# Kernel optimization log

Hardware: AMD Instinct MI355X
Metric: run time of the kernel (lower is better)

Reference implementation:

```python
import jax, jax.numpy as jnp
import numpy as np

N_NODES = 50000
N_EDGES = 400000
D_IN = 128
D_H = 128
N_CLASSES = 20
N_GRAPHS = 256
EPS_BN = 1e-5


def _lin_params(key, d_in, d_out, scale=0.05):
    kw, kb = jax.random.split(key)
    W = jax.random.normal(kw, (d_in, d_out), jnp.float32) * scale
    b = jax.random.normal(kb, (d_out,), jnp.float32) * scale
    return W, b


def setup_inputs() -> dict:
    key = jax.random.key(0)
    ks = jax.random.split(key, 20)
    inp = {
        "x": jax.random.normal(ks[0], (N_NODES, D_IN), jnp.float32),
        "edge_index": jax.random.randint(ks[1], (2, N_EDGES), 0, N_NODES, jnp.int32),
        "batch": jnp.sort(jax.random.randint(ks[2], (N_NODES,), 0, N_GRAPHS, jnp.int32)),
    }
    kidx = 3
    for li, d_in in zip((1, 2, 3), (D_IN, D_H, D_H)):
        for nm in ("q", "k", "v", "s"):
            W, b = _lin_params(ks[kidx], d_in, D_H)
            kidx += 1
            inp[f"W{nm}{li}"] = W
            inp[f"b{nm}{li}"] = b
        inp[f"gamma{li}"] = jnp.ones((D_H,), jnp.float32)
        inp[f"beta{li}"] = jnp.zeros((D_H,), jnp.float32)
    Wl, bl = _lin_params(ks[kidx], D_H, N_CLASSES)
    inp["Wlin"] = Wl
    inp["blin"] = bl
    return inp


def _segment_softmax(logits, seg, n):
    m = jax.ops.segment_max(logits, seg, num_segments=n)
    e = jnp.exp(logits - m[seg])
    s = jax.ops.segment_sum(e, seg, num_segments=n)
    return e / (s[seg] + 1e-16)


def _transformer_conv(x, src, dst, Wq, bq, Wk, bk, Wv, bv, Ws, bs):
    # heads=1, concat=True, root_weight=True (PyG TransformerConv defaults)
    q = x @ Wq + bq  # [N, d]
    k = x @ Wk + bk
    v = x @ Wv + bv
    d = q.shape[-1]
    logits = jnp.sum(q[dst] * k[src], axis=-1) / jnp.sqrt(jnp.float32(d))  # [E]
    alpha = _segment_softmax(logits, dst, x.shape[0])
    out = jax.ops.segment_sum(alpha[:, None] * v[src], dst, num_segments=x.shape[0])
    return out + x @ Ws + bs


def _batch_norm(x, gamma, beta):
    mu = jnp.mean(x, axis=0)
    var = jnp.var(x, axis=0)
    return gamma * (x - mu) * jax.lax.rsqrt(var + EPS_BN) + beta


def _global_mean_pool(x, batch, n_graphs):
    sums = jax.ops.segment_sum(x, batch, num_segments=n_graphs)
    cnt = jax.ops.segment_sum(jnp.ones((x.shape[0],), x.dtype), batch, num_segments=n_graphs)
    return sums / jnp.maximum(cnt, 1.0)[:, None]


def reference(x, edge_index, batch,
              Wq1, bq1, Wk1, bk1, Wv1, bv1, Ws1, bs1, gamma1, beta1,
              Wq2, bq2, Wk2, bk2, Wv2, bv2, Ws2, bs2, gamma2, beta2,
              Wq3, bq3, Wk3, bk3, Wv3, bv3, Ws3, bs3, gamma3, beta3,
              Wlin, blin):
    src, dst = edge_index[0], edge_index[1]
    h = _transformer_conv(x, src, dst, Wq1, bq1, Wk1, bk1, Wv1, bv1, Ws1, bs1)
    h = jax.nn.relu(_batch_norm(h, gamma1, beta1))  # dropout inactive (eval)
    h = _transformer_conv(h, src, dst, Wq2, bq2, Wk2, bk2, Wv2, bv2, Ws2, bs2)
    h = jax.nn.relu(_batch_norm(h, gamma2, beta2))
    h = _transformer_conv(h, src, dst, Wq3, bq3, Wk3, bk3, Wv3, bv3, Ws3, bs3)
    h = jax.nn.relu(_batch_norm(h, gamma3, beta3))
    g = _global_mean_pool(h, batch, N_GRAPHS)  # [G, d]
    return g @ Wlin + blin  # [G, num_classes]
```

## Files before the change

### kernel.cpp

```cpp
#include <hip/hip_runtime.h>

#define N_NODES 50000
#define N_EDGES 400000
#define DH 128
#define N_GRAPHS 256

#define SCAN_CHUNK 512
#define N_CHUNKS ((N_NODES + SCAN_CHUNK - 1) / SCAN_CHUNK)
#define ATTN_BLOCKS ((N_NODES + 15) / 16)

typedef __bf16 bf16x8 __attribute__((ext_vector_type(8)));
typedef float f32x4 __attribute__((ext_vector_type(4)));
typedef _Float16 f16x2 __attribute__((ext_vector_type(2)));
typedef _Float16 f16x8 __attribute__((ext_vector_type(8)));

#define DEV __device__ __forceinline__

#if defined(__has_builtin)
#if __has_builtin(__builtin_amdgcn_fdot2)
#define HAS_FDOT2 1
#endif
#endif

DEV float fdot2acc(f16x2 a, f16x2 b, float c) {
#ifdef HAS_FDOT2
  return __builtin_amdgcn_fdot2(a, b, c, false);
#else
  return (float)a.x * (float)b.x + (float)a.y * (float)b.y + c;
#endif
}

DEV unsigned short f2bf(float f) {
  union { float f; unsigned int i; } v; v.f = f;
  unsigned int x = v.i;
  unsigned int r = (x + 0x7fffu + ((x >> 16) & 1u)) >> 16;
  return (unsigned short)r;
}

struct WPtrs { const float* w[12]; };

__global__ void repack_kernel(WPtrs wp, unsigned short* __restrict__ WB) {
  int mat = blockIdx.y;
  int m = blockIdx.x * 256 + threadIdx.x;
  int j = m & 7;
  int lane = (m >> 3) & 63;
  int ct = (m >> 9) & 7;
  int kk = m >> 12;
  int i = kk * 32 + (lane >> 4) * 8 + j;
  int o = ct * 16 + (lane & 15);
  WB[mat * 16384 + m] = f2bf(wp.w[mat][i * 128 + o]);
}

__global__ void deg_count(const int* __restrict__ ei, int* __restrict__ deg, int E) {
  int e = blockIdx.x * 256 + threadIdx.x;
  if (e < E) atomicAdd(&deg[ei[E + e]], 1);
}

__global__ __launch_bounds__(256) void scan_sum(const int* __restrict__ deg,
                                                int* __restrict__ partials, int N) {
  __shared__ int red[256];
  int b = blockIdx.x, t = threadIdx.x;
  int base = b * SCAN_CHUNK + t * 2;
  int s = 0;
  if (base + 1 < N) { int2 v = *reinterpret_cast<const int2*>(deg + base); s = v.x + v.y; }
  else if (base < N) s = deg[base];
  red[t] = s;
  __syncthreads();
  for (int off = 128; off; off >>= 1) {
    if (t < off) red[t] += red[t + off];
    __syncthreads();
  }
  if (t == 0) partials[b] = red[0];
}

__global__ __launch_bounds__(128) void scan_partials(int* __restrict__ partials) {
  __shared__ int s[128];
  int t = threadIdx.x;
  int v = (t < N_CHUNKS) ? partials[t] : 0;
  s[t] = v;
  __syncthreads();
  for (int off = 1; off < 128; off <<= 1) {
    int o = (t >= off) ? s[t - off] : 0;
    __syncthreads();
    s[t] += o;
    __syncthreads();
  }
  if (t < N_CHUNKS) partials[t] = s[t] - v;
}

__global__ __launch_bounds__(256) void scan_apply(const int* __restrict__ deg,
                                                  const int* __restrict__ partials,
                                                  int* __restrict__ rowptr,
                                                  int* __restrict__ cursor, int N, int E) {
  __shared__ int s[256];
  int b = blockIdx.x, t = threadIdx.x;
  int base = b * SCAN_CHUNK + t * 2;
  int d0 = 0, d1 = 0;
  if (base + 1 < N) { int2 v = *reinterpret_cast<const int2*>(deg + base); d0 = v.x; d1 = v.y; }
  else if (base < N) d0 = deg[base];
  int local = d0 + d1;
  s[t] = local;
  __syncthreads();
  for (int off = 1; off < 256; off <<= 1) {
    int o = (t >= off) ? s[t - off] : 0;
    __syncthreads();
    s[t] += o;
    __syncthreads();
  }
  int offp = partials[b] + s[t] - local;
  if (base < N)     { rowptr[base] = offp;          cursor[base] = offp; }
  if (base + 1 < N) { rowptr[base + 1] = offp + d0; cursor[base + 1] = offp + d0; }
  if (b == 0 && t == 0) rowptr[N] = E;
}

__global__ void csr_scatter(const int* __restrict__ ei, int* __restrict__ cursor,
                            int* __restrict__ adj, int E) {
  int e = blockIdx.x * 256 + threadIdx.x;
  if (e < E) {
    int dst = ei[E + e];
    int pos = atomicAdd(&cursor[dst], 1);
    adj[pos] = ei[e];
  }
}

__global__ __launch_bounds__(256) void adj_sort(const int* __restrict__ rowptr,
                                                int* __restrict__ adj, int N) {
  int n = blockIdx.x * 256 + threadIdx.x;
  if (n >= N) return;
  int p0 = rowptr[n], p1 = rowptr[n + 1];
  for (int i = p0 + 1; i < p1; ++i) {
    int v = adj[i];
    int j = i - 1;
    while (j >= p0 && adj[j] > v) { adj[j + 1] = adj[j]; --j; }
    adj[j + 1] = v;
  }
}

struct GemmOut { _Float16* Y[4]; const float* bias[4]; };

#define LDP 136

__global__ __launch_bounds__(256) void gemm_proj(
    const float* __restrict__ Xf,
    const _Float16* __restrict__ Hin,
    const float* __restrict__ scale, const float* __restrict__ shift,
    const unsigned short* __restrict__ WB4,
    GemmOut go, int useBN, int N)
{
  __shared__ __align__(16) unsigned short xs[64 * LDP];

  const int t = threadIdx.x;
  const int rowBase = blockIdx.x * 64;
  const int igc = (t & 15) * 8;

  if (useBN) {
    float4 sc0 = *reinterpret_cast<const float4*>(scale + igc);
    float4 sc1 = *reinterpret_cast<const float4*>(scale + igc + 4);
    float4 sh0 = *reinterpret_cast<const float4*>(shift + igc);
    float4 sh1 = *reinterpret_cast<const float4*>(shift + igc + 4);
#pragma unroll
    for (int j = 0; j < 4; ++j) {
      int v = t + 256 * j;
      int r = v >> 4;
      int grow = rowBase + r;
      ushort4 o0 = make_ushort4(0, 0, 0, 0), o1 = make_ushort4(0, 0, 0, 0);
      if (grow < N) {
        f16x8 hv = *reinterpret_cast<const f16x8*>(Hin + (size_t)grow * 128 + igc);
        o0.x = f2bf(fmaxf((float)hv[0] * sc0.x + sh0.x, 0.f));
        o0.y = f2bf(fmaxf((float)hv[1] * sc0.y + sh0.y, 0.f));
        o0.z = f2bf(fmaxf((float)hv[2] * sc0.z + sh0.z, 0.f));
        o0.w = f2bf(fmaxf((float)hv[3] * sc0.w + sh0.w, 0.f));
        o1.x = f2bf(fmaxf((float)hv[4] * sc1.x + sh1.x, 0.f));
        o1.y = f2bf(fmaxf((float)hv[5] * sc1.y + sh1.y, 0.f));
        o1.z = f2bf(fmaxf((float)hv[6] * sc1.z + sh1.z, 0.f));
        o1.w = f2bf(fmaxf((float)hv[7] * sc1.w + sh1.w, 0.f));
      }
      *reinterpret_cast<ushort4*>(&xs[r * LDP + igc]) = o0;
      *reinterpret_cast<ushort4*>(&xs[r * LDP + igc + 4]) = o1;
    }
  } else {
#pragma unroll
    for (int j = 0; j < 4; ++j) {
      int v = t + 256 * j;
      int r = v >> 4;
      int grow = rowBase + r;
      ushort4 o0 = make_ushort4(0, 0, 0, 0), o1 = make_ushort4(0, 0, 0, 0);
      if (grow < N) {
        float4 a = *reinterpret_cast<const float4*>(Xf + (size_t)grow * 128 + igc);
        float4 b = *reinterpret_cast<const float4*>(Xf + (size_t)grow * 128 + igc + 4);
        o0.x = f2bf(a.x); o0.y = f2bf(a.y); o0.z = f2bf(a.z); o0.w = f2bf(a.w);
        o1.x = f2bf(b.x); o1.y = f2bf(b.y); o1.z = f2bf(b.z); o1.w = f2bf(b.w);
      }
      *reinterpret_cast<ushort4*>(&xs[r * LDP + igc]) = o0;
      *reinterpret_cast<ushort4*>(&xs[r * LDP + igc + 4]) = o1;
    }
  }
  __syncthreads();

  const int wave = t >> 6;
  const int lane = t & 63;
  const int ln16 = lane & 15;
  const int quad = lane >> 4;
  const int r0 = wave * 16;

  bf16x8 afrag[4];
#pragma unroll
  for (int kk = 0; kk < 4; ++kk)
    afrag[kk] = *reinterpret_cast<const bf16x8*>(&xs[(r0 + ln16) * LDP + kk * 32 + quad * 8]);

  for (int proj = 0; proj < 4; ++proj) {
    const unsigned short* __restrict__ WB = WB4 + proj * 16384;
    const float* __restrict__ bias = go.bias[proj];

    f32x4 acc[8] = {};
#pragma unroll
    for (int kk = 0; kk < 4; ++kk) {
#pragma unroll
      for (int ct = 0; ct < 8; ++ct) {
        bf16x8 b = *reinterpret_cast<const bf16x8*>(WB + ((kk * 8 + ct) * 64 + lane) * 8);
        acc[ct] = __builtin_amdgcn_mfma_f32_16x16x32_bf16(afrag[kk], b, acc[ct], 0, 0, 0);
      }
    }

    _Float16* __restrict__ Yh = go.Y[proj];
#pragma unroll
    for (int ct = 0; ct < 8; ++ct) {
      int col = ct * 16 + ln16;
      float bv = bias[col];
#pragma unroll
      for (int reg = 0; reg < 4; ++reg) {
        int grow = rowBase + r0 + quad * 4 + reg;
        if (grow < N) Yh[(size_t)grow * 128 + col] = (_Float16)(acc[ct][reg] + bv);
      }
    }
  }
}

__global__ __launch_bounds__(256) void node_attn(
    const int* __restrict__ rowptr, const int* __restrict__ adj,
    const _Float16* __restrict__ Q, const _Float16* __restrict__ K,
    const _Float16* __restrict__ V, _Float16* __restrict__ H,
    float* __restrict__ Pbuf, int N)
{
  __shared__ float lsum[16][128];
  __shared__ float lsq[16][128];
  int t = threadIdx.x;
  int w = t >> 4, lane = t & 15;
  int n = blockIdx.x * 16 + w;
  bool valid = n < N;
  int nn = valid ? n : 0;
  int p0 = 0, p1 = 0;
  if (valid) { p0 = rowptr[n]; p1 = rowptr[n + 1]; }

  f16x8 qv = *reinterpret_cast<const f16x8*>(Q + (size_t)nn * 128 + lane * 8);
  f16x2 q0 = {qv[0], qv[1]}, q1 = {qv[2], qv[3]}, q2 = {qv[4], qv[5]}, q3 = {qv[6], qv[7]};

  float m = -INFINITY, s = 0.f;
  float acc[8] = {};

  int p = p0;
  for (; p + 1 < p1; p += 2) {
    int s0 = adj[p], s1 = adj[p + 1];
    f16x8 k0 = *reinterpret_cast<const f16x8*>(K + (size_t)s0 * 128 + lane * 8);
    f16x8 k1 = *reinterpret_cast<const f16x8*>(K + (size_t)s1 * 128 + lane * 8);
    float d0 = fdot2acc(q0, (f16x2){k0[0], k0[1]},
               fdot2acc(q1, (f16x2){k0[2], k0[3]},
               fdot2acc(q2, (f16x2){k0[4], k0[5]},
               fdot2acc(q3, (f16x2){k0[6], k0[7]}, 0.f))));
    float d1 = fdot2acc(q0, (f16x2){k1[0], k1[1]},
               fdot2acc(q1, (f16x2){k1[2], k1[3]},
               fdot2acc(q2, (f16x2){k1[4], k1[5]},
               fdot2acc(q3, (f16x2){k1[6], k1[7]}, 0.f))));
#pragma unroll
    for (int off = 8; off; off >>= 1) {
      d0 += __shfl_xor(d0, off, 16);
      d1 += __shfl_xor(d1, off, 16);
    }
    float l0 = d0 * 0.08838834764831845f;
    float l1 = d1 * 0.08838834764831845f;
    float mn = fmaxf(m, fmaxf(l0, l1));
    float sc = __expf(m - mn);
    float w0 = __expf(l0 - mn);
    float w1 = __expf(l1 - mn);
    f16x8 v0 = *reinterpret_cast<const f16x8*>(V + (size_t)s0 * 128 + lane * 8);
    f16x8 v1 = *reinterpret_cast<const f16x8*>(V + (size_t)s1 * 128 + lane * 8);
#pragma unroll
    for (int i = 0; i < 8; ++i)
      acc[i] = acc[i] * sc + w0 * (float)v0[i] + w1 * (float)v1[i];
    s = s * sc + w0 + w1;
    m = mn;
  }
  if (p < p1) {
    int s0 = adj[p];
    f16x8 k0 = *reinterpret_cast<const f16x8*>(K + (size_t)s0 * 128 + lane * 8);
    float d0 = fdot2acc(q0, (f16x2){k0[0], k0[1]},
               fdot2acc(q1, (f16x2){k0[2], k0[3]},
               fdot2acc(q2, (f16x2){k0[4], k0[5]},
               fdot2acc(q3, (f16x2){k0[6], k0[7]}, 0.f))));
#pragma unroll
    for (int off = 8; off; off >>= 1) d0 += __shfl_xor(d0, off, 16);
    float l0 = d0 * 0.08838834764831845f;
    float mn = fmaxf(m, l0);
    float sc = __expf(m - mn);
    float w0 = __expf(l0 - mn);
    f16x8 v0 = *reinterpret_cast<const f16x8*>(V + (size_t)s0 * 128 + lane * 8);
#pragma unroll
    for (int i = 0; i < 8; ++i)
      acc[i] = acc[i] * sc + w0 * (float)v0[i];
    s = s * sc + w0;
    m = mn;
  }

  float h[8];
#pragma unroll
  for (int i = 0; i < 8; ++i) h[i] = 0.f;
  if (valid) {
    float inv = 1.0f / (s + 1e-16f);
    f16x8 hh = *reinterpret_cast<const f16x8*>(H + (size_t)n * 128 + lane * 8);
    f16x8 ho;
#pragma unroll
    for (int i = 0; i < 8; ++i) {
      h[i] = (float)hh[i] + acc[i] * inv;
      ho[i] = (_Float16)h[i];
    }
    *reinterpret_cast<f16x8*>(H + (size_t)n * 128 + lane * 8) = ho;
  }

#pragma unroll
  for (int i = 0; i < 8; i += 4) {
    float4 hv = make_float4(h[i], h[i + 1], h[i + 2], h[i + 3]);
    float4 h2 = make_float4(hv.x * hv.x, hv.y * hv.y, hv.z * hv.z, hv.w * hv.w);
    *reinterpret_cast<float4*>(&lsum[w][lane * 8 + i]) = hv;
    *reinterpret_cast<float4*>(&lsq[w][lane * 8 + i]) = h2;
  }
  __syncthreads();

  int f = t & 127;
  float a = 0.f;
  if (t < 128) {
#pragma unroll
    for (int n16 = 0; n16 < 16; ++n16) a += lsum[n16][f];
  } else {
#pragma unroll
    for (int n16 = 0; n16 < 16; ++n16) a += lsq[n16][f];
  }
  Pbuf[(size_t)blockIdx.x * 256 + t] = a;
}

__global__ __launch_bounds__(256) void bn_reduceA(const float* __restrict__ Pbuf,
                                                  float* __restrict__ partial) {
  int t = threadIdx.x;
  float s0 = 0.f, s1 = 0.f, s2 = 0.f, s3 = 0.f;
  int r = blockIdx.x;
  for (; r + 192 < ATTN_BLOCKS; r += 256) {
    s0 += Pbuf[(size_t)(r      ) * 256 + t];
    s1 += Pbuf[(size_t)(r +  64) * 256 + t];
    s2 += Pbuf[(size_t)(r + 128) * 256 + t];
    s3 += Pbuf[(size_t)(r + 192) * 256 + t];
  }
  for (; r < ATTN_BLOCKS; r += 64) s0 += Pbuf[(size_t)r * 256 + t];
  partial[blockIdx.x * 256 + t] = s0 + s1 + s2 + s3;
}

__global__ __launch_bounds__(256) void bn_reduceB(
    const float* __restrict__ partial,
    const float* __restrict__ gamma, const float* __restrict__ beta,
    float* __restrict__ scale, float* __restrict__ shift, int N)
{
  __shared__ float red[256];
  int t = threadIdx.x;
  float s0 = 0.f, s1 = 0.f, s2 = 0.f, s3 = 0.f;
#pragma unroll
  for (int r = 0; r < 64; r += 4) {
    s0 += partial[(r + 0) * 256 + t];
    s1 += partial[(r + 1) * 256 + t];
    s2 += partial[(r + 2) * 256 + t];
    s3 += partial[(r + 3) * 256 + t];
  }
  red[t] = s0 + s1 + s2 + s3;
  __syncthreads();
  if (t < 128) {
    float mean = red[t] / (float)N;
    float var = red[t + 128] / (float)N - mean * mean;
    var = fmaxf(var, 0.f);
    float sc = gamma[t] * rsqrtf(var + 1e-5f);
    scale[t] = sc;
    shift[t] = beta[t] - mean * sc;
  }
}

__global__ __launch_bounds__(128) void pool_graph(
    const _Float16* __restrict__ H, const float* __restrict__ scale,
    const float* __restrict__ shift, const int* __restrict__ batch,
    float* __restrict__ pooled, int N)
{
  int g = blockIdx.x;
  int f = threadIdx.x;
  int lo = 0, hi = N;
  while (lo < hi) { int mid = (lo + hi) >> 1; if (batch[mid] < g) lo = mid + 1; else hi = mid; }
  int start = lo;
  hi = N;
  while (lo < hi) { int mid = (lo + hi) >> 1; if (batch[mid] < g + 1) lo = mid + 1; else hi = mid; }
  int end = lo;
  float sc = scale[f], sh = shift[f];
  float s = 0.f;
  for (int r = start; r < end; ++r)
    s += fmaxf((float)H[(size_t)r * 128 + f] * sc + sh, 0.f);
  pooled[g * 128 + f] = s;
}

__global__ __launch_bounds__(64) void final_linear(
    const float* __restrict__ pooled, const int* __restrict__ batch,
    const float* __restrict__ Wlin, const float* __restrict__ blin,
    float* __restrict__ out, int N)
{
  int g = blockIdx.x;
  int c = threadIdx.x;
  int lo = 0, hi = N;
  while (lo < hi) { int mid = (lo + hi) >> 1; if (batch[mid] < g) lo = mid + 1; else hi = mid; }
  int start = lo;
  hi = N;
  while (lo < hi) { int mid = (lo + hi) >> 1; if (batch[mid] < g + 1) lo = mid + 1; else hi = mid; }
  float inv = 1.0f / fmaxf((float)(lo - start), 1.f);
  if (c < 20) {
    float acc = 0.f;
#pragma unroll 4
    for (int i = 0; i < 128; ++i)
      acc += pooled[g * 128 + i] * Wlin[i * 20 + c];
    out[g * 20 + c] = acc * inv + blin[c];
  }
}

extern "C" void kernel_launch(void* const* d_in, const int* in_sizes, int n_in,
                              void* d_out, int out_size, void* d_ws, size_t ws_size,
                              hipStream_t stream)
{
  const int N = N_NODES, E = N_EDGES, G = N_GRAPHS;

  const float* x = (const float*)d_in[0];
  const int* ei = (const int*)d_in[1];
  const int* batch = (const int*)d_in[2];
  const float* Wlin = (const float*)d_in[33];
  const float* blin = (const float*)d_in[34];

  char* ws = (char*)d_ws;
  size_t off = 0;
  auto alloc = [&](size_t bytes) -> void* {
    void* p = ws + off;
    off = (off + bytes + 255) & ~(size_t)255;
    return p;
  };
  unsigned short* WB = (unsigned short*)alloc(12 * 16384 * sizeof(unsigned short));
  _Float16* Qh  = (_Float16*)alloc((size_t)N * 128 * 2);
  _Float16* Kh  = (_Float16*)alloc((size_t)N * 128 * 2);
  _Float16* Vh  = (_Float16*)alloc((size_t)N * 128 * 2);
  _Float16* Hh  = (_Float16*)alloc((size_t)N * 128 * 2);
  int* deg      = (int*)alloc((size_t)N * 4);
  int* rowptr   = (int*)alloc((size_t)(N + 1) * 4);
  int* cursor   = (int*)alloc((size_t)N * 4);
  int* adj      = (int*)alloc((size_t)E * 4);
  int* partials = (int*)alloc((size_t)N_CHUNKS * 4);
  float* Pbuf   = (float*)alloc((size_t)ATTN_BLOCKS * 256 * 4);
  float* bnpart = (float*)alloc((size_t)64 * 256 * 4);
  float* scale  = (float*)alloc(128 * 4);
  float* shift  = (float*)alloc(128 * 4);
  float* pooled = (float*)alloc((size_t)G * 128 * 4);

  WPtrs wp;
  for (int L = 0; L < 3; ++L) {
    wp.w[L * 4 + 0] = (const float*)d_in[3 + L * 10 + 0];
    wp.w[L * 4 + 1] = (const float*)d_in[3 + L * 10 + 2];
    wp.w[L * 4 + 2] = (const float*)d_in[3 + L * 10 + 4];
    wp.w[L * 4 + 3] = (const float*)d_in[3 + L * 10 + 6];
  }
  repack_kernel<<<dim3(64, 12), 256, 0, stream>>>(wp, WB);

  hipMemsetAsync(deg, 0, (size_t)N * 4, stream);
  deg_count<<<(E + 255) / 256, 256, 0, stream>>>(ei, deg, E);
  scan_sum<<<N_CHUNKS, 256, 0, stream>>>(deg, partials, N);
  scan_partials<<<1, 128, 0, stream>>>(partials);
  scan_apply<<<N_CHUNKS, 256, 0, stream>>>(deg, partials, rowptr, cursor, N, E);
  csr_scatter<<<(E + 255) / 256, 256, 0, stream>>>(ei, cursor, adj, E);
  adj_sort<<<(N + 255) / 256, 256, 0, stream>>>(rowptr, adj, N);

  for (int L = 0; L < 3; ++L) {
    GemmOut go;
    go.Y[0] = Qh; go.Y[1] = Kh; go.Y[2] = Vh; go.Y[3] = Hh;
    go.bias[0] = (const float*)d_in[3 + L * 10 + 1];
    go.bias[1] = (const float*)d_in[3 + L * 10 + 3];
    go.bias[2] = (const float*)d_in[3 + L * 10 + 5];
    go.bias[3] = (const float*)d_in[3 + L * 10 + 7];
    gemm_proj<<<(N + 63) / 64, 256, 0, stream>>>(
        x, Hh, scale, shift, WB + L * 4 * 16384, go, (L > 0) ? 1 : 0, N);

    node_attn<<<ATTN_BLOCKS, 256, 0, stream>>>(rowptr, adj, Qh, Kh, Vh, Hh, Pbuf, N);

    bn_reduceA<<<64, 256, 0, stream>>>(Pbuf, bnpart);
    bn_reduceB<<<1, 256, 0, stream>>>(bnpart,
        (const float*)d_in[3 + L * 10 + 8],
        (const float*)d_in[3 + L * 10 + 9],
        scale, shift, N);

    if (L == 2) {
      pool_graph<<<G, 128, 0, stream>>>(Hh, scale, shift, batch, pooled, N);
      final_linear<<<G, 64, 0, stream>>>(pooled, batch, Wlin, blin, (float*)d_out, N);
    }
  }
}
```

Measured before the change: 523.6 us.

## Parallelize graph mean-pool over node chunks and stage adjacency sort in LDS

Replaces the per-graph serial pooling kernel, which ran one block per graph, with a chunk-parallel pass. Each 64-row block writes per-graph partial sums into one of 16 slots picked from the block index and row parity, and the final linear kernel reduces those 16 slots before the matmul. This is meant to expose more parallelism than 256 long serial loops, at the cost of an extra memset and a larger partial buffer. Correctness assumes no graph spans more than 8 consecutive chunks, about 512 nodes; a larger graph would make slots collide and overwrite partial sums. Separately, the per-node insertion sort of adjacency lists is done in shared memory when a node's degree is at most 28, to avoid repeated global read-modify-write shifts.

Result: faster. 468.7 us (-10.5%).

```diff
diff --git a/kernel.cpp b/kernel.cpp
--- a/kernel.cpp
+++ b/kernel.cpp
@@ -8,6 +8,9 @@
 #define SCAN_CHUNK 512
 #define N_CHUNKS ((N_NODES + SCAN_CHUNK - 1) / SCAN_CHUNK)
 #define ATTN_BLOCKS ((N_NODES + 15) / 16)
+#define POOL_CHUNKS ((N_NODES + 63) / 64)
+#define PSLOTS 16
+#define SORT_CAP 28
 
 typedef __bf16 bf16x8 __attribute__((ext_vector_type(8)));
 typedef float f32x4 __attribute__((ext_vector_type(4)));
@@ -125,14 +128,29 @@
 
 __global__ __launch_bounds__(256) void adj_sort(const int* __restrict__ rowptr,
                                                 int* __restrict__ adj, int N) {
-  int n = blockIdx.x * 256 + threadIdx.x;
+  __shared__ int buf[SORT_CAP * 256];
+  int t = threadIdx.x;
+  int n = blockIdx.x * 256 + t;
   if (n >= N) return;
   int p0 = rowptr[n], p1 = rowptr[n + 1];
-  for (int i = p0 + 1; i < p1; ++i) {
-    int v = adj[i];
-    int j = i - 1;
-    while (j >= p0 && adj[j] > v) { adj[j + 1] = adj[j]; --j; }
-    adj[j + 1] = v;
+  int d = p1 - p0;
+  if (d <= 1) return;
+  if (d <= SORT_CAP) {
+    for (int i = 0; i < d; ++i) buf[i * 256 + t] = adj[p0 + i];
+    for (int i = 1; i < d; ++i) {
+      int v = buf[i * 256 + t];
+      int j = i - 1;
+      while (j >= 0 && buf[j * 256 + t] > v) { buf[(j + 1) * 256 + t] = buf[j * 256 + t]; --j; }
+      buf[(j + 1) * 256 + t] = v;
+    }
+    for (int i = 0; i < d; ++i) adj[p0 + i] = buf[i * 256 + t];
+  } else {
+    for (int i = p0 + 1; i < p1; ++i) {
+      int v = adj[i];
+      int j = i - 1;
+      while (j >= p0 && adj[j] > v) { adj[j + 1] = adj[j]; --j; }
+      adj[j + 1] = v;
+    }
   }
 }
 
@@ -389,45 +407,54 @@
   }
 }
 
-__global__ __launch_bounds__(128) void pool_graph(
+__global__ __launch_bounds__(256) void pool_partial(
     const _Float16* __restrict__ H, const float* __restrict__ scale,
     const float* __restrict__ shift, const int* __restrict__ batch,
-    float* __restrict__ pooled, int N)
+    float* __restrict__ partial, int N)
 {
-  int g = blockIdx.x;
-  int f = threadIdx.x;
-  int lo = 0, hi = N;
-  while (lo < hi) { int mid = (lo + hi) >> 1; if (batch[mid] < g) lo = mid + 1; else hi = mid; }
-  int start = lo;
-  hi = N;
-  while (lo < hi) { int mid = (lo + hi) >> 1; if (batch[mid] < g + 1) lo = mid + 1; else hi = mid; }
-  int end = lo;
+  int f = threadIdx.x & 127, parity = threadIdx.x >> 7;
+  int base = blockIdx.x * 64;
+  int lim = min(base + 64, N);
   float sc = scale[f], sh = shift[f];
-  float s = 0.f;
-  for (int r = start; r < end; ++r)
-    s += fmaxf((float)H[(size_t)r * 128 + f] * sc + sh, 0.f);
-  pooled[g * 128 + f] = s;
-}
-
-__global__ __launch_bounds__(64) void final_linear(
-    const float* __restrict__ pooled, const int* __restrict__ batch,
+  int slot = ((blockIdx.x & 7) << 1) | parity;
+  int curg = -1; float s = 0.f;
+  for (int row = base + parity; row < lim; row += 2) {
+    int g = batch[row];
+    if (g != curg) {
+      if (curg >= 0) partial[(size_t)((curg << 4) | slot) * 128 + f] = s;
+      curg = g; s = 0.f;
+    }
+    s += fmaxf((float)H[(size_t)row * 128 + f] * sc + sh, 0.f);
+  }
+  if (curg >= 0) partial[(size_t)((curg << 4) | slot) * 128 + f] = s;
+}
+
+__global__ __launch_bounds__(128) void final_linear(
+    const float* __restrict__ partial, const int* __restrict__ batch,
     const float* __restrict__ Wlin, const float* __restrict__ blin,
     float* __restrict__ out, int N)
 {
+  __shared__ float pf[128];
   int g = blockIdx.x;
-  int c = threadIdx.x;
+  int t = threadIdx.x;
+  float s = 0.f;
+#pragma unroll
+  for (int sl = 0; sl < PSLOTS; ++sl)
+    s += partial[(size_t)((g << 4) | sl) * 128 + t];
+  pf[t] = s;
+  __syncthreads();
   int lo = 0, hi = N;
   while (lo < hi) { int mid = (lo + hi) >> 1; if (batch[mid] < g) lo = mid + 1; else hi = mid; }
   int start = lo;
   hi = N;
   while (lo < hi) { int mid = (lo + hi) >> 1; if (batch[mid] < g + 1) lo = mid + 1; else hi = mid; }
   float inv = 1.0f / fmaxf((float)(lo - start), 1.f);
-  if (c < 20) {
+  if (t < 20) {
     float acc = 0.f;
 #pragma unroll 4
     for (int i = 0; i < 128; ++i)
-      acc += pooled[g * 128 + i] * Wlin[i * 20 + c];
-    out[g * 20 + c] = acc * inv + blin[c];
+      acc += pf[i] * Wlin[i * 20 + t];
+    out[g * 20 + t] = acc * inv + blin[t];
   }
 }
 
@@ -464,7 +491,7 @@
   float* bnpart = (float*)alloc((size_t)64 * 256 * 4);
   float* scale  = (float*)alloc(128 * 4);
   float* shift  = (float*)alloc(128 * 4);
-  float* pooled = (float*)alloc((size_t)G * 128 * 4);
+  float* ppool  = (float*)alloc((size_t)G * PSLOTS * 128 * 4);
 
   WPtrs wp;
   for (int L = 0; L < 3; ++L) {
@@ -476,6 +503,7 @@
   repack_kernel<<<dim3(64, 12), 256, 0, stream>>>(wp, WB);
 
   hipMemsetAsync(deg, 0, (size_t)N * 4, stream);
+  hipMemsetAsync(ppool, 0, (size_t)G * PSLOTS * 128 * 4, stream);
   deg_count<<<(E + 255) / 256, 256, 0, stream>>>(ei, deg, E);
   scan_sum<<<N_CHUNKS, 256, 0, stream>>>(deg, partials, N);
   scan_partials<<<1, 128, 0, stream>>>(partials);
@@ -502,8 +530,8 @@
         scale, shift, N);
 
     if (L == 2) {
-      pool_graph<<<G, 128, 0, stream>>>(Hh, scale, shift, batch, pooled, N);
-      final_linear<<<G, 64, 0, stream>>>(pooled, batch, Wlin, blin, (float*)d_out, N);
-    }
-  }
-}
+      pool_partial<<<POOL_CHUNKS, 256, 0, stream>>>(Hh, scale, shift, batch, ppool, N);
+      final_linear<<<G, 128, 0, stream>>>(ppool, batch, Wlin, blin, (float*)d_out, N);
+    }
+  }
+}
```
